# Kernel tuning notes

Hardware: AMD Instinct MI355X
Metric: run time of the kernel (lower is better)

## Reference

```python
import jax, jax.numpy as jnp
import numpy as np

B, L, E, H, FF = 2, 2048, 1024, 16, 4096
DH = E // H
EPS = 1e-5
# NOTE: source has attn_scale = 1 / dh**(-0.5) == sqrt(dh) (multiplies, not divides)
ATTN_SCALE = float(DH) ** 0.5


def _layernorm(x, w, b):
    mu = jnp.mean(x, axis=-1, keepdims=True)
    var = jnp.mean((x - mu) ** 2, axis=-1, keepdims=True)
    return (x - mu) * jax.lax.rsqrt(var + EPS) * w + b


def setup_inputs() -> dict:
    key = jax.random.key(0)
    ks = jax.random.split(key, 8)
    s = 0.02
    return {
        "x": jax.random.normal(ks[0], (B, L, E), jnp.float32),
        "ln1_w": jnp.ones((E,), jnp.float32),
        "ln1_b": jnp.zeros((E,), jnp.float32),
        "wq": jax.random.normal(ks[1], (E, E), jnp.float32) * s,
        "bq": jnp.zeros((E,), jnp.float32),
        "wk": jax.random.normal(ks[2], (E, E), jnp.float32) * s,
        "bk": jnp.zeros((E,), jnp.float32),
        "wv": jax.random.normal(ks[3], (E, E), jnp.float32) * s,
        "bv": jnp.zeros((E,), jnp.float32),
        "wo": jax.random.normal(ks[4], (E, E), jnp.float32) * s,
        "bo": jnp.zeros((E,), jnp.float32),
        "ln2_w": jnp.ones((E,), jnp.float32),
        "ln2_b": jnp.zeros((E,), jnp.float32),
        "wu": jax.random.normal(ks[5], (E, FF), jnp.float32) * s,
        "bu": jnp.zeros((FF,), jnp.float32),
        "wd": jax.random.normal(ks[6], (FF, E), jnp.float32) * s,
        "bd": jnp.zeros((E,), jnp.float32),
    }


def reference(x, ln1_w, ln1_b, wq, bq, wk, bk, wv, bv, wo, bo,
              ln2_w, ln2_b, wu, bu, wd, bd):
    # --- attention block (pre-LN, manual softmax attention) ---
    xn = _layernorm(x, ln1_w, ln1_b)                       # [B,L,E]
    q = (xn @ wq + bq).reshape(B, L, H, DH)
    k = (xn @ wk + bk).reshape(B, L, H, DH)
    v = (xn @ wv + bv).reshape(B, L, H, DH)
    score = jnp.einsum("blhd,bmhd->bhlm", q, k) * ATTN_SCALE  # [B,H,L,L]
    attn = jax.nn.softmax(score, axis=-1)
    ctx = jnp.einsum("bhlm,bmhd->blhd", attn, v).reshape(B, L, E)
    hidden = x + (ctx @ wo + bo)
    # --- FFN block (pre-LN, GELU) ---
    hn = _layernorm(hidden, ln2_w, ln2_b)
    up = jax.nn.gelu(hn @ wu + bu, approximate=False)      # [B,L,F]
    down = up @ wd + bd
    return hidden + down
```

## Files before the change

kernel.cpp:

```cpp
#include <hip/hip_runtime.h>
#include <stdint.h>


typedef __attribute__((ext_vector_type(8))) short short8;
typedef __attribute__((ext_vector_type(4))) float floatx4;

extern "C" __device__ float __ocml_native_exp2_f32(float);
#define EXP2(x) __ocml_native_exp2_f32(x)

#define MFMA_BF16(a, b, c) __builtin_amdgcn_mfma_f32_16x16x32_bf16((a), (b), (c), 0, 0, 0)

__device__ __forceinline__ unsigned short f2bf(float f) {
  union { float f; unsigned int u; } v; v.f = f;
  unsigned int r = v.u + 0x7FFFu + ((v.u >> 16) & 1u);
  return (unsigned short)(r >> 16);
}

__device__ __forceinline__ unsigned int f2u(float f) {
  union { float f; unsigned int u; } v; v.f = f; return v.u;
}

__device__ __forceinline__ void gl_lds16(const unsigned short* g, unsigned short* l) {
  __builtin_amdgcn_global_load_lds(
      (const __attribute__((address_space(1))) unsigned int*)g,
      (__attribute__((address_space(3))) unsigned int*)l, 16, 0, 0);
}

template <int MODE, int BN>
__global__ __launch_bounds__(256)
void gemm_bt(const unsigned short* __restrict__ A,
             const unsigned short* __restrict__ Bt,
             const float* __restrict__ bias,
             void* __restrict__ outp,
             const float* __restrict__ res,
             int K,
             void* __restrict__ out2, void* __restrict__ out3,
             const float* __restrict__ bias2, const float* __restrict__ bias3) {
  constexpr int BM = 128, BK = 64;
  constexpr int MI = (BN == 128) ? 4 : 2;
  constexpr int NI = 4;
  __shared__ __align__(16) unsigned short As[BM * BK];
  __shared__ __align__(16) unsigned short Bs[BN * BK];
  const int tid = threadIdx.x;
  const int wave = tid >> 6, lane = tid & 63, l16 = lane & 15, quad = lane >> 4;
  const int m0 = blockIdx.y * BM, n0 = blockIdx.x * BN;
  const int wm = (BN == 128) ? (wave >> 1) * 64 : wave * 32;
  const int wn = (BN == 128) ? (wave & 1) * 64 : 0;
  const int sw = l16 & 7;
  const int sl0 = (quad ^ sw) << 3;
  const int sl1 = sl0 ^ 32;

  floatx4 acc[MI][NI] = {};

  for (int k0 = 0; k0 < K; k0 += BK) {
    __syncthreads();
#pragma unroll
    for (int c = 0; c < (BM * BK) / 2048; ++c) {
      const int e = (c * 256 + tid) * 8;
      const int row = e >> 6, c8 = (e >> 3) & 7;
      gl_lds16(A + (size_t)(m0 + row) * K + k0 + ((c8 ^ (row & 7)) << 3), &As[e]);
    }
#pragma unroll
    for (int c = 0; c < (BN * BK) / 2048; ++c) {
      const int e = (c * 256 + tid) * 8;
      const int row = e >> 6, c8 = (e >> 3) & 7;
      gl_lds16(Bt + (size_t)(n0 + row) * K + k0 + ((c8 ^ (row & 7)) << 3), &Bs[e]);
    }
    __syncthreads();

    short8 af0[MI], af1[MI], bf0[NI], bf1[NI];
#pragma unroll
    for (int i = 0; i < MI; ++i) {
      af0[i] = *(const short8*)&As[(wm + i * 16 + l16) * BK + sl0];
      af1[i] = *(const short8*)&As[(wm + i * 16 + l16) * BK + sl1];
    }
#pragma unroll
    for (int i = 0; i < NI; ++i) {
      bf0[i] = *(const short8*)&Bs[(wn + i * 16 + l16) * BK + sl0];
      bf1[i] = *(const short8*)&Bs[(wn + i * 16 + l16) * BK + sl1];
    }
#pragma unroll
    for (int mi = 0; mi < MI; ++mi)
#pragma unroll
      for (int ni = 0; ni < NI; ++ni) {
        acc[mi][ni] = MFMA_BF16(af0[mi], bf0[ni], acc[mi][ni]);
        acc[mi][ni] = MFMA_BF16(af1[mi], bf1[ni], acc[mi][ni]);
      }
  }

  const int seg = (MODE == 0) ? (n0 >> 10) : 0;
  const float* bptr = bias;
  if constexpr (MODE == 0) bptr = (seg == 0) ? bias : (seg == 1 ? bias2 : bias3);

  float bcol[NI];
#pragma unroll
  for (int ni = 0; ni < NI; ++ni) {
    const int n = n0 + wn + ni * 16 + l16;
    bcol[ni] = bptr[(MODE == 0) ? (n & 1023) : n];
  }

#pragma unroll
  for (int mi = 0; mi < MI; ++mi) {
#pragma unroll
    for (int r = 0; r < 4; ++r) {
      const int m = m0 + wm + mi * 16 + quad * 4 + r;
#pragma unroll
      for (int ni = 0; ni < NI; ++ni) {
        const int n = n0 + wn + ni * 16 + l16;
        const float c = acc[mi][ni][r] + bcol[ni];
        if constexpr (MODE == 0) {
          const int b_ = m >> 11, l = m & 2047, hd = n & 1023;
          const size_t idx =
              ((size_t)((b_ * 16 + (hd >> 6)) * 2048 + l)) * 64 + (hd & 63);
          if (seg == 0)       ((unsigned short*)outp)[idx] = f2bf(c * 11.5415603270f);
          else if (seg == 1)  ((unsigned short*)out2)[idx] = f2bf(c);
          else                ((unsigned short*)out3)[idx] = f2bf(c);
        } else if constexpr (MODE == 1) {
          ((float*)outp)[(size_t)m * 1024 + n] = res[(size_t)m * 1024 + n] + c;
        } else if constexpr (MODE == 2) {
          const float g = 0.5f * c * (1.0f + erff(c * 0.70710678118654752f));
          ((unsigned short*)outp)[(size_t)m * 4096 + n] = f2bf(g);
        } else {
          ((float*)outp)[(size_t)m * 1024 + n] = res[(size_t)m * 1024 + n] + c;
        }
      }
    }
  }
}

__global__ __launch_bounds__(256)
void layernorm_kernel(const float* __restrict__ x, const float* __restrict__ w,
                      const float* __restrict__ b, unsigned short* __restrict__ out) {
  const int row = blockIdx.x, tid = threadIdx.x;
  const int wave = tid >> 6, lane = tid & 63;
  const float4 v = ((const float4*)(x + (size_t)row * 1024))[tid];
  float s = v.x + v.y + v.z + v.w;
  float s2 = v.x * v.x + v.y * v.y + v.z * v.z + v.w * v.w;
#pragma unroll
  for (int off = 32; off > 0; off >>= 1) {
    s += __shfl_down(s, off);
    s2 += __shfl_down(s2, off);
  }
  __shared__ float red[8];
  if (lane == 0) { red[wave] = s; red[4 + wave] = s2; }
  __syncthreads();
  const float ts = red[0] + red[1] + red[2] + red[3];
  const float ts2 = red[4] + red[5] + red[6] + red[7];
  const float mu = ts * (1.0f / 1024.0f);
  const float var = ts2 * (1.0f / 1024.0f) - mu * mu;
  const float rs = rsqrtf(var + 1e-5f);
  const float4 wv = ((const float4*)w)[tid];
  const float4 bv = ((const float4*)b)[tid];
  ushort4 o;
  o.x = f2bf((v.x - mu) * rs * wv.x + bv.x);
  o.y = f2bf((v.y - mu) * rs * wv.y + bv.y);
  o.z = f2bf((v.z - mu) * rs * wv.z + bv.z);
  o.w = f2bf((v.w - mu) * rs * wv.w + bv.w);
  ((ushort4*)(out + (size_t)row * 1024))[tid] = o;
}

__global__ __launch_bounds__(256)
void transpose_cast4(const float* __restrict__ s0, const float* __restrict__ s1,
                     const float* __restrict__ s2, const float* __restrict__ s3,
                     unsigned short* __restrict__ dst) {
  __shared__ float tile[32][33];
  const int z = blockIdx.z;
  const float* in = (z == 0) ? s0 : (z == 1) ? s1 : (z == 2) ? s2 : s3;
  unsigned short* out = dst + (size_t)z * 1024 * 1024;
  const int tx = threadIdx.x, ty = threadIdx.y;
  const int c0 = blockIdx.x * 32, r0 = blockIdx.y * 32;
#pragma unroll
  for (int i = 0; i < 4; ++i)
    tile[ty + 8 * i][tx] = in[(size_t)(r0 + ty + 8 * i) * 1024 + c0 + tx];
  __syncthreads();
#pragma unroll
  for (int i = 0; i < 4; ++i)
    out[(size_t)(c0 + ty + 8 * i) * 1024 + r0 + tx] = f2bf(tile[tx][ty + 8 * i]);
}

__global__ __launch_bounds__(256)
void transpose_cast(const float* __restrict__ in, unsigned short* __restrict__ out,
                    int R, int C) {
  __shared__ float tile[32][33];
  const int tx = threadIdx.x, ty = threadIdx.y;
  const int c0 = blockIdx.x * 32, r0 = blockIdx.y * 32;
#pragma unroll
  for (int i = 0; i < 4; ++i)
    tile[ty + 8 * i][tx] = in[(size_t)(r0 + ty + 8 * i) * C + c0 + tx];
  __syncthreads();
#pragma unroll
  for (int i = 0; i < 4; ++i)
    out[(size_t)(c0 + ty + 8 * i) * R + r0 + tx] = f2bf(tile[tx][ty + 8 * i]);
}

__global__ __launch_bounds__(256)
void transpose_bf16(const unsigned short* __restrict__ in,
                    unsigned short* __restrict__ out, int R, int C) {
  __shared__ unsigned short tile[32][33];
  const size_t hoff = (size_t)blockIdx.z * R * C;
  in += hoff; out += hoff;
  const int tx = threadIdx.x, ty = threadIdx.y;
  const int c0 = blockIdx.x * 32, r0 = blockIdx.y * 32;
#pragma unroll
  for (int i = 0; i < 4; ++i)
    tile[ty + 8 * i][tx] = in[(size_t)(r0 + ty + 8 * i) * C + c0 + tx];
  __syncthreads();
#pragma unroll
  for (int i = 0; i < 4; ++i)
    out[(size_t)(c0 + ty + 8 * i) * R + r0 + tx] = tile[tx][ty + 8 * i];
}

__global__ __launch_bounds__(256)
void flash_attn(const unsigned short* __restrict__ q,
                const unsigned short* __restrict__ k,
                const unsigned short* __restrict__ v,
                unsigned short* __restrict__ ctx) {
  __shared__ __align__(16) unsigned short Ks[2][64 * 64];
  __shared__ __align__(16) unsigned short Vs[2][64 * 64];
  __shared__ __align__(16) unsigned short Ps[4][2][16 * 72];
  const int bh = blockIdx.y, qt = blockIdx.x;
  const int tid = threadIdx.x, wave = tid >> 6, lane = tid & 63;
  const int l16 = lane & 15, quad = lane >> 4;
  const unsigned short* kb = k + (size_t)bh * 2048 * 64;
  const unsigned short* vb = v + (size_t)bh * 64 * 2048;

  int qrow[2];
  short8 qf0[2], qf1[2];
#pragma unroll
  for (int g = 0; g < 2; ++g) {
    qrow[g] = qt * 128 + g * 64 + wave * 16 + l16;
    const unsigned short* qp = q + (size_t)bh * 2048 * 64 + (size_t)qrow[g] * 64;
    qf0[g] = *(const short8*)(qp + quad * 8);
    qf1[g] = *(const short8*)(qp + 32 + quad * 8);
  }

  floatx4 O[2][4] = {};
  float m_run[2] = {-1e30f, -1e30f}, l_run[2] = {0.f, 0.f};

  auto stage = [&](int t, int bufi) {
    const int kv0 = t * 64;
#pragma unroll
    for (int c = 0; c < 2; ++c) {
      const int e = (c * 256 + tid) * 8;
      const int r = e >> 6, ch = (e >> 3) & 7;
      const int sc = ((ch ^ (r & 7)) << 3);
      gl_lds16(kb + (size_t)(kv0 + r) * 64 + sc, &Ks[bufi][e]);
      gl_lds16(vb + (size_t)r * 2048 + kv0 + sc, &Vs[bufi][e]);
    }
  };
  stage(0, 0);

  const int sw = l16 & 7;
  const int sl0 = (quad ^ sw) << 3, sl1 = sl0 ^ 32;

  for (int t = 0; t < 32; ++t) {
    __syncthreads();
    const int bufi = t & 1;
    if (t + 1 < 32) stage(t + 1, bufi ^ 1);

    floatx4 st[2][4];
#pragma unroll
    for (int nt = 0; nt < 4; ++nt) {
      const int r0 = (nt * 16 + l16) * 64;
      const short8 kf0 = *(const short8*)&Ks[bufi][r0 + sl0];
      const short8 kf1 = *(const short8*)&Ks[bufi][r0 + sl1];
#pragma unroll
      for (int g = 0; g < 2; ++g) {
        floatx4 z = {};
        z = MFMA_BF16(kf0, qf0[g], z);
        z = MFMA_BF16(kf1, qf1[g], z);
        st[g][nt] = z;
      }
    }

    short8 pf0[2], pf1[2];
#pragma unroll
    for (int g = 0; g < 2; ++g) {
      float mx = st[g][0][0];
#pragma unroll
      for (int nt = 0; nt < 4; ++nt)
#pragma unroll
        for (int r = 0; r < 4; ++r) mx = fmaxf(mx, st[g][nt][r]);
      mx = fmaxf(mx, __shfl_xor(mx, 16));
      mx = fmaxf(mx, __shfl_xor(mx, 32));
      const float m_new = fmaxf(m_run[g], mx);
      const float alpha = EXP2(m_run[g] - m_new);
      m_run[g] = m_new;

      float rsum = 0.f;
#pragma unroll
      for (int nt = 0; nt < 4; ++nt) {
        const float p0 = EXP2(st[g][nt][0] - m_new);
        const float p1 = EXP2(st[g][nt][1] - m_new);
        const float p2 = EXP2(st[g][nt][2] - m_new);
        const float p3 = EXP2(st[g][nt][3] - m_new);
        rsum += (p0 + p1) + (p2 + p3);
        uint2 pk;
        pk.x = __builtin_amdgcn_perm(f2u(p1), f2u(p0), 0x07060302u);
        pk.y = __builtin_amdgcn_perm(f2u(p3), f2u(p2), 0x07060302u);
        *(uint2*)&Ps[wave][g][l16 * 72 + nt * 16 + quad * 4] = pk;
      }
      rsum += __shfl_xor(rsum, 16);
      rsum += __shfl_xor(rsum, 32);
      l_run[g] = l_run[g] * alpha + rsum;

#pragma unroll
      for (int nt = 0; nt < 4; ++nt) {
        O[g][nt][0] *= alpha; O[g][nt][1] *= alpha;
        O[g][nt][2] *= alpha; O[g][nt][3] *= alpha;
      }
      pf0[g] = *(const short8*)&Ps[wave][g][l16 * 72 + quad * 8];
      pf1[g] = *(const short8*)&Ps[wave][g][l16 * 72 + 32 + quad * 8];
    }

#pragma unroll
    for (int nt = 0; nt < 4; ++nt) {
      const int r0 = (nt * 16 + l16) * 64;
      const short8 vf0 = *(const short8*)&Vs[bufi][r0 + sl0];
      const short8 vf1 = *(const short8*)&Vs[bufi][r0 + sl1];
#pragma unroll
      for (int g = 0; g < 2; ++g) {
        O[g][nt] = MFMA_BF16(vf0, pf0[g], O[g][nt]);
        O[g][nt] = MFMA_BF16(vf1, pf1[g], O[g][nt]);
      }
    }
  }

  const int b_ = bh >> 4, h = bh & 15;
#pragma unroll
  for (int g = 0; g < 2; ++g) {
    const float inv = 1.0f / l_run[g];
    unsigned short* op = ctx + ((size_t)(b_ * 2048) + qrow[g]) * 1024 + h * 64;
#pragma unroll
    for (int nt = 0; nt < 4; ++nt) {
      ushort4 o4;
      o4.x = f2bf(O[g][nt][0] * inv);
      o4.y = f2bf(O[g][nt][1] * inv);
      o4.z = f2bf(O[g][nt][2] * inv);
      o4.w = f2bf(O[g][nt][3] * inv);
      *(ushort4*)(op + nt * 16 + quad * 4) = o4;
    }
  }
}

extern "C" void kernel_launch(void* const* d_in, const int* in_sizes, int n_in,
                              void* d_out, int out_size, void* d_ws, size_t ws_size,
                              hipStream_t stream) {
  const float* x     = (const float*)d_in[0];
  const float* ln1_w = (const float*)d_in[1];
  const float* ln1_b = (const float*)d_in[2];
  const float* wq    = (const float*)d_in[3];
  const float* bq    = (const float*)d_in[4];
  const float* wk    = (const float*)d_in[5];
  const float* bk    = (const float*)d_in[6];
  const float* wv    = (const float*)d_in[7];
  const float* bv    = (const float*)d_in[8];
  const float* wo    = (const float*)d_in[9];
  const float* bo    = (const float*)d_in[10];
  const float* ln2_w = (const float*)d_in[11];
  const float* ln2_b = (const float*)d_in[12];
  const float* wu    = (const float*)d_in[13];
  const float* bu    = (const float*)d_in[14];
  const float* wd    = (const float*)d_in[15];
  const float* bd    = (const float*)d_in[16];

  char* W = (char*)d_ws;
  const size_t MB = 1ull << 20;
  unsigned short* wqkvT = (unsigned short*)(W + 0 * MB);
  unsigned short* woT   = (unsigned short*)(W + 6 * MB);
  unsigned short* wuT   = (unsigned short*)(W + 8 * MB);
  unsigned short* wdT   = (unsigned short*)(W + 16 * MB);
  unsigned short* xn    = (unsigned short*)(W + 24 * MB);
  unsigned short* qb    = (unsigned short*)(W + 32 * MB);
  unsigned short* kb    = (unsigned short*)(W + 40 * MB);
  unsigned short* vb    = (unsigned short*)(W + 48 * MB);
  unsigned short* cx    = (unsigned short*)(W + 56 * MB);
  float*          hid   = (float*)(W + 64 * MB);
  unsigned short* up    = (unsigned short*)(W + 24 * MB);

  const dim3 tb(32, 8);
  transpose_cast4<<<dim3(32, 32, 4), tb, 0, stream>>>(wq, wk, wv, wo, wqkvT);
  transpose_cast<<<dim3(128, 32), tb, 0, stream>>>(wu, wuT, 1024, 4096);
  transpose_cast<<<dim3(32, 128), tb, 0, stream>>>(wd, wdT, 4096, 1024);

  layernorm_kernel<<<4096, 256, 0, stream>>>(x, ln1_w, ln1_b, xn);
  gemm_bt<0, 128><<<dim3(24, 32), 256, 0, stream>>>(
      xn, wqkvT, bq, qb, nullptr, 1024, kb, cx, bk, bv);
  transpose_bf16<<<dim3(2, 64, 32), tb, 0, stream>>>(cx, vb, 2048, 64);
  flash_attn<<<dim3(16, 32), 256, 0, stream>>>(qb, kb, vb, cx);
  gemm_bt<1, 64><<<dim3(16, 32), 256, 0, stream>>>(
      cx, woT, bo, hid, x, 1024, nullptr, nullptr, nullptr, nullptr);

  layernorm_kernel<<<4096, 256, 0, stream>>>(hid, ln2_w, ln2_b, cx);
  gemm_bt<2, 128><<<dim3(32, 32), 256, 0, stream>>>(
      cx, wuT, bu, up, nullptr, 1024, nullptr, nullptr, nullptr, nullptr);
  gemm_bt<3, 64><<<dim3(16, 32), 256, 0, stream>>>(
      up, wdT, bd, d_out, hid, 4096, nullptr, nullptr, nullptr, nullptr);
}
```

Measured before the change: 393.9 us.

## Rewrite flash attention with 32x32 MFMA, register-resident P and lazy rescale

The attention kernel moves from 16x16x32 MFMA tiles to 32x32x16 tiles, with each wave owning 32 query rows. The V transpose writes a permuted column order so that the softmax probabilities from the score MFMA can be packed directly into B operands, which removes the LDS round trip for P. It also skips the running-max rescale of O and l unless the new max exceeds the old one by more than 8 (in log2 units) for some lane, cutting exp and multiply work. The cost is more accumulator registers per wave, and the deferred rescale assumes bounded growth of the exponent, which relies on fp32 headroom.

```diff
diff --git a/kernel.cpp b/kernel.cpp
--- a/kernel.cpp
+++ b/kernel.cpp
@@ -4,11 +4,13 @@
 
 typedef __attribute__((ext_vector_type(8))) short short8;
 typedef __attribute__((ext_vector_type(4))) float floatx4;
+typedef __attribute__((ext_vector_type(16))) float floatx16;
 
 extern "C" __device__ float __ocml_native_exp2_f32(float);
 #define EXP2(x) __ocml_native_exp2_f32(x)
 
 #define MFMA_BF16(a, b, c) __builtin_amdgcn_mfma_f32_16x16x32_bf16((a), (b), (c), 0, 0, 0)
+#define MFMA32(a, b, c) __builtin_amdgcn_mfma_f32_32x32x16_bf16((a), (b), (c), 0, 0, 0)
 
 __device__ __forceinline__ unsigned short f2bf(float f) {
   union { float f; unsigned int u; } v; v.f = f;
@@ -18,6 +20,12 @@
 
 __device__ __forceinline__ unsigned int f2u(float f) {
   union { float f; unsigned int u; } v; v.f = f; return v.u;
+}
+
+__device__ __forceinline__ short8 pack4(unsigned a, unsigned b, unsigned c, unsigned d) {
+  union { unsigned u[4]; short8 s; } v;
+  v.u[0] = a; v.u[1] = b; v.u[2] = c; v.u[3] = d;
+  return v.s;
 }
 
 __device__ __forceinline__ void gl_lds16(const unsigned short* g, unsigned short* l) {
@@ -205,9 +213,10 @@
   for (int i = 0; i < 4; ++i)
     tile[ty + 8 * i][tx] = in[(size_t)(r0 + ty + 8 * i) * C + c0 + tx];
   __syncthreads();
-#pragma unroll
-  for (int i = 0; i < 4; ++i)
-    out[(size_t)(c0 + ty + 8 * i) * R + r0 + tx] = tile[tx][ty + 8 * i];
+  const int txp = (tx & ~12) | ((tx & 4) << 1) | ((tx & 8) >> 1);
+#pragma unroll
+  for (int i = 0; i < 4; ++i)
+    out[(size_t)(c0 + ty + 8 * i) * R + r0 + txp] = tile[tx][ty + 8 * i];
 }
 
 __global__ __launch_bounds__(256)
@@ -217,25 +226,24 @@
                 unsigned short* __restrict__ ctx) {
   __shared__ __align__(16) unsigned short Ks[2][64 * 64];
   __shared__ __align__(16) unsigned short Vs[2][64 * 64];
-  __shared__ __align__(16) unsigned short Ps[4][2][16 * 72];
   const int bh = blockIdx.y, qt = blockIdx.x;
   const int tid = threadIdx.x, wave = tid >> 6, lane = tid & 63;
-  const int l16 = lane & 15, quad = lane >> 4;
+  const int lo = lane & 31, hi = lane >> 5, sw7 = lo & 7;
   const unsigned short* kb = k + (size_t)bh * 2048 * 64;
   const unsigned short* vb = v + (size_t)bh * 64 * 2048;
 
-  int qrow[2];
-  short8 qf0[2], qf1[2];
-#pragma unroll
-  for (int g = 0; g < 2; ++g) {
-    qrow[g] = qt * 128 + g * 64 + wave * 16 + l16;
-    const unsigned short* qp = q + (size_t)bh * 2048 * 64 + (size_t)qrow[g] * 64;
-    qf0[g] = *(const short8*)(qp + quad * 8);
-    qf1[g] = *(const short8*)(qp + 32 + quad * 8);
-  }
-
-  floatx4 O[2][4] = {};
-  float m_run[2] = {-1e30f, -1e30f}, l_run[2] = {0.f, 0.f};
+  const int qrow = qt * 128 + wave * 32 + lo;
+  const unsigned short* qp = q + ((size_t)bh * 2048 + qrow) * 64;
+  short8 qf[4];
+#pragma unroll
+  for (int kq = 0; kq < 4; ++kq) qf[kq] = *(const short8*)(qp + kq * 16 + hi * 8);
+
+  int co[4];
+#pragma unroll
+  for (int j = 0; j < 4; ++j) co[j] = ((j * 2 + hi) ^ sw7) << 3;
+
+  floatx16 O0 = {}, O1 = {};
+  float m_run = -1e30f, l_run = 0.f;
 
   auto stage = [&](int t, int bufi) {
     const int kv0 = t * 64;
@@ -250,96 +258,77 @@
   };
   stage(0, 0);
 
-  const int sw = l16 & 7;
-  const int sl0 = (quad ^ sw) << 3, sl1 = sl0 ^ 32;
-
   for (int t = 0; t < 32; ++t) {
     __syncthreads();
     const int bufi = t & 1;
     if (t + 1 < 32) stage(t + 1, bufi ^ 1);
 
-    floatx4 st[2][4];
-#pragma unroll
-    for (int nt = 0; nt < 4; ++nt) {
-      const int r0 = (nt * 16 + l16) * 64;
-      const short8 kf0 = *(const short8*)&Ks[bufi][r0 + sl0];
-      const short8 kf1 = *(const short8*)&Ks[bufi][r0 + sl1];
-#pragma unroll
-      for (int g = 0; g < 2; ++g) {
-        floatx4 z = {};
-        z = MFMA_BF16(kf0, qf0[g], z);
-        z = MFMA_BF16(kf1, qf1[g], z);
-        st[g][nt] = z;
-      }
-    }
-
-    short8 pf0[2], pf1[2];
-#pragma unroll
-    for (int g = 0; g < 2; ++g) {
-      float mx = st[g][0][0];
-#pragma unroll
-      for (int nt = 0; nt < 4; ++nt)
-#pragma unroll
-        for (int r = 0; r < 4; ++r) mx = fmaxf(mx, st[g][nt][r]);
-      mx = fmaxf(mx, __shfl_xor(mx, 16));
-      mx = fmaxf(mx, __shfl_xor(mx, 32));
-      const float m_new = fmaxf(m_run[g], mx);
-      const float alpha = EXP2(m_run[g] - m_new);
-      m_run[g] = m_new;
-
-      float rsum = 0.f;
-#pragma unroll
-      for (int nt = 0; nt < 4; ++nt) {
-        const float p0 = EXP2(st[g][nt][0] - m_new);
-        const float p1 = EXP2(st[g][nt][1] - m_new);
-        const float p2 = EXP2(st[g][nt][2] - m_new);
-        const float p3 = EXP2(st[g][nt][3] - m_new);
-        rsum += (p0 + p1) + (p2 + p3);
-        uint2 pk;
-        pk.x = __builtin_amdgcn_perm(f2u(p1), f2u(p0), 0x07060302u);
-        pk.y = __builtin_amdgcn_perm(f2u(p3), f2u(p2), 0x07060302u);
-        *(uint2*)&Ps[wave][g][l16 * 72 + nt * 16 + quad * 4] = pk;
-      }
-      rsum += __shfl_xor(rsum, 16);
-      rsum += __shfl_xor(rsum, 32);
-      l_run[g] = l_run[g] * alpha + rsum;
-
-#pragma unroll
-      for (int nt = 0; nt < 4; ++nt) {
-        O[g][nt][0] *= alpha; O[g][nt][1] *= alpha;
-        O[g][nt][2] *= alpha; O[g][nt][3] *= alpha;
-      }
-      pf0[g] = *(const short8*)&Ps[wave][g][l16 * 72 + quad * 8];
-      pf1[g] = *(const short8*)&Ps[wave][g][l16 * 72 + 32 + quad * 8];
-    }
-
-#pragma unroll
-    for (int nt = 0; nt < 4; ++nt) {
-      const int r0 = (nt * 16 + l16) * 64;
-      const short8 vf0 = *(const short8*)&Vs[bufi][r0 + sl0];
-      const short8 vf1 = *(const short8*)&Vs[bufi][r0 + sl1];
-#pragma unroll
-      for (int g = 0; g < 2; ++g) {
-        O[g][nt] = MFMA_BF16(vf0, pf0[g], O[g][nt]);
-        O[g][nt] = MFMA_BF16(vf1, pf1[g], O[g][nt]);
-      }
-    }
-  }
-
-  const int b_ = bh >> 4, h = bh & 15;
-#pragma unroll
-  for (int g = 0; g < 2; ++g) {
-    const float inv = 1.0f / l_run[g];
-    unsigned short* op = ctx + ((size_t)(b_ * 2048) + qrow[g]) * 1024 + h * 64;
-#pragma unroll
-    for (int nt = 0; nt < 4; ++nt) {
-      ushort4 o4;
-      o4.x = f2bf(O[g][nt][0] * inv);
-      o4.y = f2bf(O[g][nt][1] * inv);
-      o4.z = f2bf(O[g][nt][2] * inv);
-      o4.w = f2bf(O[g][nt][3] * inv);
-      *(ushort4*)(op + nt * 16 + quad * 4) = o4;
-    }
+    const unsigned short* Kb = &Ks[bufi][0];
+    const unsigned short* Vb = &Vs[bufi][0];
+
+    floatx16 st0 = {}, st1 = {};
+#pragma unroll
+    for (int kq = 0; kq < 4; ++kq) {
+      const short8 kf0 = *(const short8*)&Kb[lo * 64 + co[kq]];
+      const short8 kf1 = *(const short8*)&Kb[(32 + lo) * 64 + co[kq]];
+      st0 = MFMA32(kf0, qf[kq], st0);
+      st1 = MFMA32(kf1, qf[kq], st1);
+    }
+
+    float mx = fmaxf(st0[0], st1[0]);
+#pragma unroll
+    for (int r = 1; r < 16; ++r) mx = fmaxf(mx, fmaxf(st0[r], st1[r]));
+    mx = fmaxf(mx, __shfl_xor(mx, 32));
+    if (!__all(mx - m_run <= 8.0f)) {
+      const float m_new = fmaxf(m_run, mx);
+      const float alpha = EXP2(m_run - m_new);
+      m_run = m_new;
+      l_run *= alpha;
+#pragma unroll
+      for (int r = 0; r < 16; ++r) { O0[r] *= alpha; O1[r] *= alpha; }
+    }
+    float rsum = 0.f;
+#pragma unroll
+    for (int r = 0; r < 16; ++r) {
+      st0[r] = EXP2(st0[r] - m_run);
+      st1[r] = EXP2(st1[r] - m_run);
+      rsum += st0[r] + st1[r];
+    }
+    rsum += __shfl_xor(rsum, 32);
+    l_run += rsum;
+
+    unsigned pw0[8], pw1[8];
+#pragma unroll
+    for (int i = 0; i < 8; ++i) {
+      pw0[i] = __builtin_amdgcn_perm(f2u(st0[2 * i + 1]), f2u(st0[2 * i]), 0x07060302u);
+      pw1[i] = __builtin_amdgcn_perm(f2u(st1[2 * i + 1]), f2u(st1[2 * i]), 0x07060302u);
+    }
+    const short8 pf[4] = { pack4(pw0[0], pw0[1], pw0[2], pw0[3]),
+                           pack4(pw0[4], pw0[5], pw0[6], pw0[7]),
+                           pack4(pw1[0], pw1[1], pw1[2], pw1[3]),
+                           pack4(pw1[4], pw1[5], pw1[6], pw1[7]) };
+
+#pragma unroll
+    for (int s = 0; s < 4; ++s) {
+      const short8 vf0 = *(const short8*)&Vb[lo * 64 + co[s]];
+      const short8 vf1 = *(const short8*)&Vb[(32 + lo) * 64 + co[s]];
+      O0 = MFMA32(vf0, pf[s], O0);
+      O1 = MFMA32(vf1, pf[s], O1);
+    }
+  }
+
+  const int b_ = bh >> 4, h_ = bh & 15;
+  const float inv = 1.0f / l_run;
+  unsigned short* op = ctx + ((size_t)(b_ * 2048) + qrow) * 1024 + h_ * 64;
+#pragma unroll
+  for (int rq = 0; rq < 4; ++rq) {
+    ushort4 a4, b4;
+    a4.x = f2bf(O0[rq * 4 + 0] * inv); a4.y = f2bf(O0[rq * 4 + 1] * inv);
+    a4.z = f2bf(O0[rq * 4 + 2] * inv); a4.w = f2bf(O0[rq * 4 + 3] * inv);
+    *(ushort4*)(op + rq * 8 + hi * 4) = a4;
+    b4.x = f2bf(O1[rq * 4 + 0] * inv); b4.y = f2bf(O1[rq * 4 + 1] * inv);
+    b4.z = f2bf(O1[rq * 4 + 2] * inv); b4.w = f2bf(O1[rq * 4 + 3] * inv);
+    *(ushort4*)(op + 32 + rq * 8 + hi * 4) = b4;
   }
 }
 
```

Result: faster. 378.8 us (-3.8%).
